# Kernel tuning notes

Measured on AMD Instinct MI355X. Metric: run time of the kernel, lower is better.

Reference implementation:

```python
import jax, jax.numpy as jnp
import numpy as np

N, D_IN, D_OUT = 10000, 256, 256


def setup_inputs() -> dict:
    key = jax.random.key(0)
    k1, k2, k3, k4 = jax.random.split(key, 4)
    # xavier_uniform with gain=1.414 (as in the torch module)
    def xavier(k, shape, gain=1.414):
        fan_in, fan_out = shape[0], shape[1]
        bound = gain * np.sqrt(6.0 / (fan_in + fan_out))
        return jax.random.uniform(k, shape, jnp.float32, -bound, bound)
    return {
        "input": jax.random.normal(k1, (N, D_IN), jnp.float32),
        "adj": jax.random.randint(k2, (N, N), 0, 2, jnp.int32),  # binary dense adjacency
        "M": N,
        "W": xavier(k3, (D_IN, D_OUT)),
        "b": jnp.zeros((D_OUT,), jnp.float32),
        "a": xavier(k4, (D_OUT, 1)),
    }


def reference(input, adj, M, W, b, a):
    # h = tanh(X W + b); values used for attention logits
    h = jnp.tanh(input @ W + b)          # [N, F]
    inp = input @ W                      # [N, F] (values to aggregate)
    e = (h @ a)[:, 0]                    # [N] per-node logit
    # original also drops neighbors whose h row sums to exactly 0
    valid = (jnp.sum(h, axis=1) != 0)    # [N]
    mask = (adj[:M] > 0) & valid[None, :]  # [M, N]
    neg = jnp.asarray(-1e30, h.dtype)
    scores = jnp.where(mask, e[None, :], neg)           # [M, N]
    m = jnp.max(scores, axis=1, keepdims=True)
    w = jnp.where(mask, jnp.exp(scores - m), 0.0)       # masked exp
    denom = jnp.sum(w, axis=1, keepdims=True)
    att = w / jnp.maximum(denom, 1e-30)  # rows with no neighbors -> all zeros (matches torch zeros init)
    # dropout is identity in eval mode (training=False)
    return att @ inp                     # [M, F]
```

## Files before the change

### kernel.cpp

```cpp
#include <hip/hip_runtime.h>
#include <hip/hip_bf16.h>
#include <cstdint>
#include <cstddef>

#define NN      10000
#define DD      256
#define KSTEPS  313
#define MB2     79
#define KSPLIT  6

typedef __bf16 bf16x8 __attribute__((ext_vector_type(8)));
typedef float  f32x4  __attribute__((ext_vector_type(4)));

#define XG_OFF   0ull
#define XG_SIZE  (32ull * 10000 * 16)
#define WG_OFF   (XG_OFF + XG_SIZE)
#define WG_SIZE  (32ull * 256 * 16)
#define INP_OFF  (WG_OFF + WG_SIZE)
#define INP_SIZE (10000ull * 256 * 4)
#define E_OFF    (INP_OFF + INP_SIZE)
#define E_SIZE   (10016ull * 4)
#define HS_OFF   (E_OFF + E_SIZE)
#define HS_SIZE  (10016ull * 4)
#define GM_OFF   (HS_OFF + HS_SIZE)
#define GM_SIZE  (256ull)
#define YG_OFF   (GM_OFF + GM_SIZE)
#define YG_SIZE  (318ull * 1088 * 16)
#define PN_OFF   (YG_OFF + YG_SIZE)
#define PN_SIZE  ((size_t)KSPLIT * 10000 * 272 * 4)

__device__ __forceinline__ void gl_lds16(const void* g, void* lds) {
    __builtin_amdgcn_global_load_lds(
        (const __attribute__((address_space(1))) unsigned int*)g,
        (__attribute__((address_space(3))) unsigned int*)lds,
        16, 0, 0);
}

__global__ __launch_bounds__(256) void k_prep(const float* __restrict__ X,
                                              bf16x8* __restrict__ XG,
                                              const float* __restrict__ W,
                                              bf16x8* __restrict__ WG,
                                              unsigned int* __restrict__ gmaxU) {
    int b = blockIdx.x;
    if (b < 1250) {
        int idx = b * 256 + threadIdx.x;
        int row = idx >> 5;
        int q   = idx & 31;
        const float* src = X + row * 256 + q * 8;
        bf16x8 v;
#pragma unroll
        for (int j = 0; j < 8; ++j) v[j] = (__bf16)src[j];
        XG[q * 10000 + row] = v;
    } else {
        int e = (b - 1250) * 256 + threadIdx.x;
        int q = e >> 8;
        int n = e & 255;
        bf16x8 v;
#pragma unroll
        for (int j = 0; j < 8; ++j) v[j] = (__bf16)W[(q * 8 + j) * 256 + n];
        WG[e] = v;
        if (b == 1250 && threadIdx.x == 0) *gmaxU = 0u;
    }
}

__global__ __launch_bounds__(256) void k_gemm1(const bf16x8* __restrict__ XG,
                                               const bf16x8* __restrict__ WG,
                                               const float* __restrict__ bvec,
                                               const float* __restrict__ avec,
                                               float* __restrict__ inp,
                                               float* __restrict__ evec,
                                               float* __restrict__ hsumv,
                                               unsigned int* __restrict__ gmaxU) {
    __shared__ bf16x8 Ash[320];
    __shared__ bf16x8 Bsh[1024];
    __shared__ float ePart[4][80];
    __shared__ float hPart[4][80];
    int tid = threadIdx.x, wid = tid >> 6, lane = tid & 63;
    int l15 = lane & 15, l4 = lane >> 4;
    int mb = blockIdx.x;

    f32x4 acc[4][5];
#pragma unroll
    for (int c = 0; c < 4; ++c)
#pragma unroll
        for (int rt = 0; rt < 5; ++rt) acc[c][rt] = f32x4{0.f, 0.f, 0.f, 0.f};

    for (int kb = 0; kb < 8; ++kb) {
        for (int rr = wid; rr < 5; rr += 4) {
            int c = rr * 64 + lane;
            int g = c / 80, r = c - g * 80;
            gl_lds16(XG + ((kb * 4 + g) * 10000 + mb * 80 + r), (char*)Ash + rr * 1024);
        }
        for (int rr = wid; rr < 16; rr += 4)
            gl_lds16(WG + kb * 1024 + rr * 64 + lane, (char*)Bsh + rr * 1024);
        __syncthreads();

        bf16x8 af[5];
#pragma unroll
        for (int rt = 0; rt < 5; ++rt) af[rt] = Ash[l4 * 80 + rt * 16 + l15];
#pragma unroll
        for (int c = 0; c < 4; ++c) {
            bf16x8 bf = Bsh[l4 * 256 + (wid * 4 + c) * 16 + l15];
#pragma unroll
            for (int rt = 0; rt < 5; ++rt)
                acc[c][rt] = __builtin_amdgcn_mfma_f32_16x16x32_bf16(af[rt], bf, acc[c][rt], 0, 0, 0);
        }
        __syncthreads();
    }

    float pe[5][4], ph[5][4];
#pragma unroll
    for (int rt = 0; rt < 5; ++rt)
#pragma unroll
        for (int rg = 0; rg < 4; ++rg) { pe[rt][rg] = 0.f; ph[rt][rg] = 0.f; }

#pragma unroll
    for (int c = 0; c < 4; ++c) {
        int col = (wid * 4 + c) * 16 + l15;
        float av = avec[col];
        float bv = bvec[col];
#pragma unroll
        for (int rt = 0; rt < 5; ++rt) {
#pragma unroll
            for (int rg = 0; rg < 4; ++rg) {
                int row = mb * 80 + rt * 16 + l4 * 4 + rg;
                float v = acc[c][rt][rg];
                inp[row * 256 + col] = v;
                float h = tanhf(v + bv);
                pe[rt][rg] += h * av;
                ph[rt][rg] += h;
            }
        }
    }
#pragma unroll
    for (int rt = 0; rt < 5; ++rt) {
#pragma unroll
        for (int rg = 0; rg < 4; ++rg) {
            float se = pe[rt][rg], sh = ph[rt][rg];
#pragma unroll
            for (int m = 1; m < 16; m <<= 1) {
                se += __shfl_xor(se, m);
                sh += __shfl_xor(sh, m);
            }
            if (l15 == 0) {
                int lr = rt * 16 + l4 * 4 + rg;
                ePart[wid][lr] = se;
                hPart[wid][lr] = sh;
            }
        }
    }
    __syncthreads();
    if (tid < 80) {
        float e = ePart[0][tid] + ePart[1][tid] + ePart[2][tid] + ePart[3][tid];
        float h = hPart[0][tid] + hPart[1][tid] + hPart[2][tid] + hPart[3][tid];
        evec[mb * 80 + tid] = e;
        hsumv[mb * 80 + tid] = h;
        ePart[0][tid] = (h != 0.0f) ? e : -3.0e38f;
    }
    __syncthreads();
    if (tid == 0) {
        float m = -3.0e38f;
        for (int i = 0; i < 80; ++i) m = fmaxf(m, ePart[0][i]);
        if (m > -2.9e38f) {
            unsigned int b = __float_as_uint(m);
            unsigned int u = (b & 0x80000000u) ? ~b : (b | 0x80000000u);
            atomicMax(gmaxU, u);
        }
    }
}

__global__ __launch_bounds__(256) void k_build_yg(const float* __restrict__ inp,
                                                  const float* __restrict__ evec,
                                                  const float* __restrict__ hsumv,
                                                  const unsigned int* __restrict__ gmaxU,
                                                  bf16x8* __restrict__ YG) {
    __shared__ float gsh[32];
    int kb = blockIdx.x;
    if (threadIdx.x < 32) {
        unsigned int gu = *gmaxU;
        float gmax = 0.0f;
        if (gu != 0u)
            gmax = (gu & 0x80000000u) ? __uint_as_float(gu ^ 0x80000000u)
                                      : __uint_as_float(~gu);
        int k = kb * 32 + threadIdx.x;
        float g = 0.0f;
        if (k < NN && hsumv[k] != 0.0f) g = expf(evec[k] - gmax);
        gsh[threadIdx.x] = g;
    }
    __syncthreads();
    for (int c = threadIdx.x; c < 1088; c += 256) {
        int gq = c / 272, n = c - gq * 272;
        int j0 = gq * 8;
        bf16x8 v;
#pragma unroll
        for (int j = 0; j < 8; ++j) {
            int k = kb * 32 + j0 + j;
            float val = 0.0f;
            if (k < NN) {
                float gk = gsh[j0 + j];
                if (n < 256) val = gk * inp[k * 256 + n];
                else if (n == 256) val = gk;
            }
            v[j] = (__bf16)val;
        }
        YG[kb * 1088 + c] = v;
    }
}

__device__ __forceinline__ bf16x8 cvt_adj(int4 a, int4 b) {
    union { bf16x8 v; unsigned int u[4]; } r;
    r.u[0] = (a.x > 0 ? 0x3F80u : 0u) | (a.y > 0 ? 0x3F800000u : 0u);
    r.u[1] = (a.z > 0 ? 0x3F80u : 0u) | (a.w > 0 ? 0x3F800000u : 0u);
    r.u[2] = (b.x > 0 ? 0x3F80u : 0u) | (b.y > 0 ? 0x3F800000u : 0u);
    r.u[3] = (b.z > 0 ? 0x3F80u : 0u) | (b.w > 0 ? 0x3F800000u : 0u);
    return r.v;
}

__global__ __launch_bounds__(256, 2) void k_attn_gemm(const int* __restrict__ adj,
                                                      const bf16x8* __restrict__ YG,
                                                      float* __restrict__ pnum) {
    __shared__ int    Ash[2][4096];
    __shared__ bf16x8 Bsh[2][1088];
    int tid = threadIdx.x, wid = tid >> 6, lane = tid & 63;
    int l15 = lane & 15, l4 = lane >> 4;

    int orig = blockIdx.x;
    const int nwg = MB2 * KSPLIT, q = nwg >> 3, r = nwg & 7;
    int x = orig & 7, o = orig >> 3;
    int logical = (x < r ? x * (q + 1) : r * (q + 1) + (x - r) * q) + o;
    int kc = logical / MB2, mb = logical % MB2;
    int s0 = (kc * KSTEPS) / KSPLIT, s1 = ((kc + 1) * KSTEPS) / KSPLIT;

    const int* aSrc[4];
    int aLim[4];
#pragma unroll
    for (int i = 0; i < 4; ++i) {
        int c = (wid + i * 4) * 64 + lane;
        int row = c >> 3;
        int p = c & 7;
        int ck4 = (p ^ (row & 7)) * 4;
        int grow = min(mb * 128 + row, NN - 1);
        aSrc[i] = adj + (size_t)grow * 10000 + ck4;
        aLim[i] = 9996 - ck4;
    }

    f32x4 acc[2][17];
#pragma unroll
    for (int t = 0; t < 2; ++t)
#pragma unroll
        for (int ct = 0; ct < 17; ++ct) acc[t][ct] = f32x4{0.f, 0.f, 0.f, 0.f};

    auto stageA = [&](int sTile, int bufIdx) {
        int kk = sTile * 32;
        char* dst = (char*)&Ash[bufIdx][0];
#pragma unroll
        for (int i = 0; i < 4; ++i)
            gl_lds16(aSrc[i] + min(kk, aLim[i]), dst + (wid + i * 4) * 1024);
    };
    auto stageB = [&](int sTile, int bufIdx) {
        const bf16x8* src = YG + (size_t)sTile * 1088;
        char* dst = (char*)&Bsh[bufIdx][0];
#pragma unroll
        for (int i = 0; i < 5; ++i) {
            int rr = wid + i * 4;
            if (rr < 17) gl_lds16(src + rr * 64 + lane, dst + rr * 1024);
        }
    };

    int xr = l15 & 7;
    int p0 = (2 * l4) ^ xr;
    int rowA0 = wid * 32 + l15;

    stageA(s0, 0);
    stageB(s0, 0);
    __syncthreads();

    int buf = 0;
    for (int s = s0; s < s1; ++s) {
        if (s + 1 < s1) {
            stageA(s + 1, buf ^ 1);
            stageB(s + 1, buf ^ 1);
        }
        const int* ab = &Ash[buf][0];
        int4 v00 = *(const int4*)(ab + rowA0 * 32 + p0 * 4);
        int4 v01 = *(const int4*)(ab + rowA0 * 32 + (p0 ^ 1) * 4);
        int4 v10 = *(const int4*)(ab + (rowA0 + 16) * 32 + p0 * 4);
        int4 v11 = *(const int4*)(ab + (rowA0 + 16) * 32 + (p0 ^ 1) * 4);
        bf16x8 fa0 = cvt_adj(v00, v01);
        bf16x8 fa1 = cvt_adj(v10, v11);
#pragma unroll
        for (int ct = 0; ct < 17; ++ct) {
            bf16x8 fb = Bsh[buf][l4 * 272 + ct * 16 + l15];
            acc[0][ct] = __builtin_amdgcn_mfma_f32_16x16x32_bf16(fa0, fb, acc[0][ct], 0, 0, 0);
            acc[1][ct] = __builtin_amdgcn_mfma_f32_16x16x32_bf16(fa1, fb, acc[1][ct], 0, 0, 0);
        }
        __syncthreads();
        buf ^= 1;
    }

    float* base = pnum + (size_t)kc * 10000 * 272;
    int r0 = mb * 128 + wid * 32;
#pragma unroll
    for (int t = 0; t < 2; ++t) {
#pragma unroll
        for (int ct = 0; ct < 17; ++ct) {
            int col = ct * 16 + l15;
#pragma unroll
            for (int rg = 0; rg < 4; ++rg) {
                int row = r0 + t * 16 + l4 * 4 + rg;
                if (row < NN) base[(size_t)row * 272 + col] = acc[t][ct][rg];
            }
        }
    }
}

__global__ __launch_bounds__(256) void k_finalize(const float* __restrict__ pnum,
                                                  float* __restrict__ out) {
    int idx = blockIdx.x * 256 + threadIdx.x;
    int i = idx >> 6, q = idx & 63;
    float4 sv = {0.f, 0.f, 0.f, 0.f};
    float den = 0.f;
#pragma unroll
    for (int kc = 0; kc < KSPLIT; ++kc) {
        const float* row = pnum + ((size_t)kc * 10000 + i) * 272;
        float4 v = ((const float4*)row)[q];
        sv.x += v.x; sv.y += v.y; sv.z += v.z; sv.w += v.w;
        den += row[256];
    }
    float r = 1.0f / fmaxf(den, 1e-30f);
    float4 o;
    o.x = sv.x * r; o.y = sv.y * r; o.z = sv.z * r; o.w = sv.w * r;
    ((float4*)(out + (size_t)i * 256))[q] = o;
}

extern "C" void kernel_launch(void* const* d_in, const int* in_sizes, int n_in,
                              void* d_out, int out_size, void* d_ws, size_t ws_size,
                              hipStream_t stream) {
    const float* X    = (const float*)d_in[0];
    const int*   adj  = (const int*)d_in[1];
    const float* W    = (const float*)d_in[3];
    const float* bvec = (const float*)d_in[4];
    const float* avec = (const float*)d_in[5];
    float* out = (float*)d_out;

    char* ws = (char*)d_ws;
    bf16x8* XG   = (bf16x8*)(ws + XG_OFF);
    bf16x8* WG   = (bf16x8*)(ws + WG_OFF);
    float*  inp  = (float*)(ws + INP_OFF);
    float*  evec = (float*)(ws + E_OFF);
    float*  hsv  = (float*)(ws + HS_OFF);
    unsigned int* gmaxU = (unsigned int*)(ws + GM_OFF);
    bf16x8* YG   = (bf16x8*)(ws + YG_OFF);
    float*  pnum = (float*)(ws + PN_OFF);

    k_prep<<<1282, 256, 0, stream>>>(X, XG, W, WG, gmaxU);
    k_gemm1<<<125, 256, 0, stream>>>(XG, WG, bvec, avec, inp, evec, hsv, gmaxU);
    k_build_yg<<<318, 256, 0, stream>>>(inp, evec, hsv, gmaxU, YG);
    k_attn_gemm<<<MB2 * KSPLIT, 256, 0, stream>>>(adj, YG, pnum);
    k_finalize<<<2500, 256, 0, stream>>>(pnum, out);
}
```

Before: 174.8 us.

## Fuse softmax weighting into GEMM1 epilogue and use atomic split-K reduction

Drops the global-max stabilisation and computes exp(e) directly in the first GEMM epilogue, writing the weighted bf16 values operand straight into the packed layout and removing the separate build kernel and intermediate buffers. The split-K partial sums are now accumulated with float atomicAdd into a single zeroed numerator buffer instead of six partial slabs, which shrinks the finalize read. This trades memory traffic and a launch for scattered 2-byte stores, many atomics, and reliance on tanh bounding the logits to avoid overflow.

```diff
diff --git a/kernel.cpp b/kernel.cpp
--- a/kernel.cpp
+++ b/kernel.cpp
@@ -16,18 +16,10 @@
 #define XG_SIZE  (32ull * 10000 * 16)
 #define WG_OFF   (XG_OFF + XG_SIZE)
 #define WG_SIZE  (32ull * 256 * 16)
-#define INP_OFF  (WG_OFF + WG_SIZE)
-#define INP_SIZE (10000ull * 256 * 4)
-#define E_OFF    (INP_OFF + INP_SIZE)
-#define E_SIZE   (10016ull * 4)
-#define HS_OFF   (E_OFF + E_SIZE)
-#define HS_SIZE  (10016ull * 4)
-#define GM_OFF   (HS_OFF + HS_SIZE)
-#define GM_SIZE  (256ull)
-#define YG_OFF   (GM_OFF + GM_SIZE)
+#define YG_OFF   (WG_OFF + WG_SIZE)
 #define YG_SIZE  (318ull * 1088 * 16)
-#define PN_OFF   (YG_OFF + YG_SIZE)
-#define PN_SIZE  ((size_t)KSPLIT * 10000 * 272 * 4)
+#define NUM_OFF  (YG_OFF + YG_SIZE)
+#define NUM_SIZE (10000ull * 260 * 4)
 
 __device__ __forceinline__ void gl_lds16(const void* g, void* lds) {
     __builtin_amdgcn_global_load_lds(
@@ -40,7 +32,7 @@
                                               bf16x8* __restrict__ XG,
                                               const float* __restrict__ W,
                                               bf16x8* __restrict__ WG,
-                                              unsigned int* __restrict__ gmaxU) {
+                                              bf16x8* __restrict__ YG) {
     int b = blockIdx.x;
     if (b < 1250) {
         int idx = b * 256 + threadIdx.x;
@@ -51,7 +43,7 @@
 #pragma unroll
         for (int j = 0; j < 8; ++j) v[j] = (__bf16)src[j];
         XG[q * 10000 + row] = v;
-    } else {
+    } else if (b < 1282) {
         int e = (b - 1250) * 256 + threadIdx.x;
         int q = e >> 8;
         int n = e & 255;
@@ -59,7 +51,12 @@
 #pragma unroll
         for (int j = 0; j < 8; ++j) v[j] = (__bf16)W[(q * 8 + j) * 256 + n];
         WG[e] = v;
-        if (b == 1250 && threadIdx.x == 0) *gmaxU = 0u;
+    } else {
+        bf16x8 z;
+#pragma unroll
+        for (int j = 0; j < 8; ++j) z[j] = (__bf16)0.0f;
+        for (int c = threadIdx.x; c < 1088; c += 256)
+            YG[312 * 1088 + c] = z;
     }
 }
 
@@ -67,14 +64,12 @@
                                                const bf16x8* __restrict__ WG,
                                                const float* __restrict__ bvec,
                                                const float* __restrict__ avec,
-                                               float* __restrict__ inp,
-                                               float* __restrict__ evec,
-                                               float* __restrict__ hsumv,
-                                               unsigned int* __restrict__ gmaxU) {
+                                               bf16x8* __restrict__ YG) {
     __shared__ bf16x8 Ash[320];
     __shared__ bf16x8 Bsh[1024];
     __shared__ float ePart[4][80];
     __shared__ float hPart[4][80];
+    __shared__ float gsh[80];
     int tid = threadIdx.x, wid = tid >> 6, lane = tid & 63;
     int l15 = lane & 15, l4 = lane >> 4;
     int mb = blockIdx.x;
@@ -123,10 +118,7 @@
         for (int rt = 0; rt < 5; ++rt) {
 #pragma unroll
             for (int rg = 0; rg < 4; ++rg) {
-                int row = mb * 80 + rt * 16 + l4 * 4 + rg;
-                float v = acc[c][rt][rg];
-                inp[row * 256 + col] = v;
-                float h = tanhf(v + bv);
+                float h = tanhf(acc[c][rt][rg] + bv);
                 pe[rt][rg] += h * av;
                 ph[rt][rg] += h;
             }
@@ -153,57 +145,30 @@
     if (tid < 80) {
         float e = ePart[0][tid] + ePart[1][tid] + ePart[2][tid] + ePart[3][tid];
         float h = hPart[0][tid] + hPart[1][tid] + hPart[2][tid] + hPart[3][tid];
-        evec[mb * 80 + tid] = e;
-        hsumv[mb * 80 + tid] = h;
-        ePart[0][tid] = (h != 0.0f) ? e : -3.0e38f;
+        gsh[tid] = (h != 0.0f) ? expf(e) : 0.0f;
     }
     __syncthreads();
-    if (tid == 0) {
-        float m = -3.0e38f;
-        for (int i = 0; i < 80; ++i) m = fmaxf(m, ePart[0][i]);
-        if (m > -2.9e38f) {
-            unsigned int b = __float_as_uint(m);
-            unsigned int u = (b & 0x80000000u) ? ~b : (b | 0x80000000u);
-            atomicMax(gmaxU, u);
-        }
-    }
-}
-
-__global__ __launch_bounds__(256) void k_build_yg(const float* __restrict__ inp,
-                                                  const float* __restrict__ evec,
-                                                  const float* __restrict__ hsumv,
-                                                  const unsigned int* __restrict__ gmaxU,
-                                                  bf16x8* __restrict__ YG) {
-    __shared__ float gsh[32];
-    int kb = blockIdx.x;
-    if (threadIdx.x < 32) {
-        unsigned int gu = *gmaxU;
-        float gmax = 0.0f;
-        if (gu != 0u)
-            gmax = (gu & 0x80000000u) ? __uint_as_float(gu ^ 0x80000000u)
-                                      : __uint_as_float(~gu);
-        int k = kb * 32 + threadIdx.x;
-        float g = 0.0f;
-        if (k < NN && hsumv[k] != 0.0f) g = expf(evec[k] - gmax);
-        gsh[threadIdx.x] = g;
-    }
-    __syncthreads();
-    for (int c = threadIdx.x; c < 1088; c += 256) {
-        int gq = c / 272, n = c - gq * 272;
-        int j0 = gq * 8;
-        bf16x8 v;
-#pragma unroll
-        for (int j = 0; j < 8; ++j) {
-            int k = kb * 32 + j0 + j;
-            float val = 0.0f;
-            if (k < NN) {
-                float gk = gsh[j0 + j];
-                if (n < 256) val = gk * inp[k * 256 + n];
-                else if (n == 256) val = gk;
-            }
-            v[j] = (__bf16)val;
-        }
-        YG[kb * 1088 + c] = v;
+
+    __bf16* Yh = (__bf16*)YG;
+#pragma unroll
+    for (int c = 0; c < 4; ++c) {
+        int col = (wid * 4 + c) * 16 + l15;
+#pragma unroll
+        for (int rt = 0; rt < 5; ++rt) {
+#pragma unroll
+            for (int rg = 0; rg < 4; ++rg) {
+                int rl = rt * 16 + l4 * 4 + rg;
+                int row = mb * 80 + rl;
+                float val = gsh[rl] * acc[c][rt][rg];
+                size_t idx = ((size_t)(row >> 5) * 1088 + ((row >> 3) & 3) * 272 + col) * 8 + (row & 7);
+                Yh[idx] = (__bf16)val;
+            }
+        }
+    }
+    if (tid < 80) {
+        int row = mb * 80 + tid;
+        size_t idx = ((size_t)(row >> 5) * 1088 + ((row >> 3) & 3) * 272 + 256) * 8 + (row & 7);
+        Yh[idx] = (__bf16)gsh[tid];
     }
 }
 
@@ -218,7 +183,7 @@
 
 __global__ __launch_bounds__(256, 2) void k_attn_gemm(const int* __restrict__ adj,
                                                       const bf16x8* __restrict__ YG,
-                                                      float* __restrict__ pnum) {
+                                                      float* __restrict__ num) {
     __shared__ int    Ash[2][4096];
     __shared__ bf16x8 Bsh[2][1088];
     int tid = threadIdx.x, wid = tid >> 6, lane = tid & 63;
@@ -298,38 +263,33 @@
         buf ^= 1;
     }
 
-    float* base = pnum + (size_t)kc * 10000 * 272;
     int r0 = mb * 128 + wid * 32;
 #pragma unroll
     for (int t = 0; t < 2; ++t) {
 #pragma unroll
         for (int ct = 0; ct < 17; ++ct) {
             int col = ct * 16 + l15;
-#pragma unroll
-            for (int rg = 0; rg < 4; ++rg) {
-                int row = r0 + t * 16 + l4 * 4 + rg;
-                if (row < NN) base[(size_t)row * 272 + col] = acc[t][ct][rg];
-            }
-        }
-    }
-}
-
-__global__ __launch_bounds__(256) void k_finalize(const float* __restrict__ pnum,
+            if (col < 257) {
+#pragma unroll
+                for (int rg = 0; rg < 4; ++rg) {
+                    int row = r0 + t * 16 + l4 * 4 + rg;
+                    if (row < NN) atomicAdd(num + (size_t)row * 260 + col, acc[t][ct][rg]);
+                }
+            }
+        }
+    }
+}
+
+__global__ __launch_bounds__(256) void k_finalize(const float* __restrict__ num,
                                                   float* __restrict__ out) {
     int idx = blockIdx.x * 256 + threadIdx.x;
     int i = idx >> 6, q = idx & 63;
-    float4 sv = {0.f, 0.f, 0.f, 0.f};
-    float den = 0.f;
-#pragma unroll
-    for (int kc = 0; kc < KSPLIT; ++kc) {
-        const float* row = pnum + ((size_t)kc * 10000 + i) * 272;
-        float4 v = ((const float4*)row)[q];
-        sv.x += v.x; sv.y += v.y; sv.z += v.z; sv.w += v.w;
-        den += row[256];
-    }
+    const float4* nr = (const float4*)(num + (size_t)i * 260);
+    float4 v = nr[q];
+    float den = num[(size_t)i * 260 + 256];
     float r = 1.0f / fmaxf(den, 1e-30f);
     float4 o;
-    o.x = sv.x * r; o.y = sv.y * r; o.z = sv.z * r; o.w = sv.w * r;
+    o.x = v.x * r; o.y = v.y * r; o.z = v.z * r; o.w = v.w * r;
     ((float4*)(out + (size_t)i * 256))[q] = o;
 }
 
@@ -344,18 +304,14 @@
     float* out = (float*)d_out;
 
     char* ws = (char*)d_ws;
-    bf16x8* XG   = (bf16x8*)(ws + XG_OFF);
-    bf16x8* WG   = (bf16x8*)(ws + WG_OFF);
-    float*  inp  = (float*)(ws + INP_OFF);
-    float*  evec = (float*)(ws + E_OFF);
-    float*  hsv  = (float*)(ws + HS_OFF);
-    unsigned int* gmaxU = (unsigned int*)(ws + GM_OFF);
-    bf16x8* YG   = (bf16x8*)(ws + YG_OFF);
-    float*  pnum = (float*)(ws + PN_OFF);
-
-    k_prep<<<1282, 256, 0, stream>>>(X, XG, W, WG, gmaxU);
-    k_gemm1<<<125, 256, 0, stream>>>(XG, WG, bvec, avec, inp, evec, hsv, gmaxU);
-    k_build_yg<<<318, 256, 0, stream>>>(inp, evec, hsv, gmaxU, YG);
-    k_attn_gemm<<<MB2 * KSPLIT, 256, 0, stream>>>(adj, YG, pnum);
-    k_finalize<<<2500, 256, 0, stream>>>(pnum, out);
-}
+    bf16x8* XG  = (bf16x8*)(ws + XG_OFF);
+    bf16x8* WG  = (bf16x8*)(ws + WG_OFF);
+    bf16x8* YG  = (bf16x8*)(ws + YG_OFF);
+    float*  num = (float*)(ws + NUM_OFF);
+
+    hipMemsetAsync(ws + NUM_OFF, 0, NUM_SIZE, stream);
+    k_prep<<<1283, 256, 0, stream>>>(X, XG, W, WG, YG);
+    k_gemm1<<<125, 256, 0, stream>>>(XG, WG, bvec, avec, YG);
+    k_attn_gemm<<<MB2 * KSPLIT, 256, 0, stream>>>(adj, YG, num);
+    k_finalize<<<2500, 256, 0, stream>>>(num, out);
+}
```

Measured after the change: 225.3 us. 1.29x slower.
